# Kernel tuning notes

Hardware: AMD Instinct MI355X
Metric: run time of the kernel (lower is better)

The kernel has to match this reference:

```python
import jax, jax.numpy as jnp
import numpy as np

N, E, T = 32768, 262144, 262144
DN, DE = 128, 128
EPS = 1e-5  # torch LayerNorm default eps


def layer_norm(x, g, b):
    m = jnp.mean(x, axis=-1, keepdims=True)
    v = jnp.mean((x - m) ** 2, axis=-1, keepdims=True)
    return (x - m) * jax.lax.rsqrt(v + EPS) * g + b


def setup_inputs() -> dict:
    key = jax.random.key(0)
    ks = jax.random.split(key, 16)
    node_embedding = jax.random.normal(ks[0], (N, DN), dtype=jnp.float32)
    edge_embedding = jax.random.normal(ks[1], (E, DE), dtype=jnp.float32)
    i = jax.random.randint(ks[2], (E,), 0, N)
    j = jax.random.randint(ks[3], (E,), 0, N)
    index_i = jax.random.randint(ks[4], (T,), 0, N)
    index_j = jax.random.randint(ks[5], (T,), 0, N)
    index_k = jax.random.randint(ks[6], (T,), 0, N)
    index_ji = jax.random.randint(ks[7], (T,), 0, E)
    index_kj = jax.random.randint(ks[8], (T,), 0, E)
    d3 = 3 * DN + 2 * DE
    W2 = jax.random.normal(ks[9], (2 * DE, DN), dtype=jnp.float32) / np.sqrt(DN)
    b2 = jnp.zeros((2 * DE,), dtype=jnp.float32)
    W3 = jax.random.normal(ks[10], (2 * DE, d3), dtype=jnp.float32) / np.sqrt(d3)
    b3 = jnp.zeros((2 * DE,), dtype=jnp.float32)
    g_c2 = jnp.ones((2 * DE,), jnp.float32); be_c2 = jnp.zeros((2 * DE,), jnp.float32)
    g_c3 = jnp.ones((2 * DE,), jnp.float32); be_c3 = jnp.zeros((2 * DE,), jnp.float32)
    g_c2_2 = jnp.ones((DE,), jnp.float32); be_c2_2 = jnp.zeros((DE,), jnp.float32)
    g_c3_2 = jnp.ones((DE,), jnp.float32); be_c3_2 = jnp.zeros((DE,), jnp.float32)
    return dict(node_embedding=node_embedding, edge_embedding=edge_embedding,
                i=i, j=j, index_i=index_i, index_j=index_j, index_k=index_k,
                index_ji=index_ji, index_kj=index_kj,
                W2=W2, b2=b2, W3=W3, b3=b3,
                g_c2=g_c2, be_c2=be_c2, g_c3=g_c3, be_c3=be_c3,
                g_c2_2=g_c2_2, be_c2_2=be_c2_2, g_c3_2=g_c3_2, be_c3_2=be_c3_2)


def reference(node_embedding, edge_embedding, i, j, index_i, index_j, index_k,
              index_ji, index_kj, W2, b2, W3, b3,
              g_c2, be_c2, g_c3, be_c3, g_c2_2, be_c2_2, g_c3_2, be_c3_2):
    num_edges = edge_embedding.shape[0]
    # --- c2 branch: per-edge elementwise product of endpoint node embeddings ---
    c2 = node_embedding[i] * node_embedding[j]                      # [E, Dn]
    c2 = layer_norm(c2 @ W2.T + b2, g_c2, be_c2)                    # [E, 2De]
    c2_filter, c2_core = jnp.split(c2, 2, axis=1)
    c2_emb = layer_norm(jax.nn.sigmoid(c2_filter) * jnp.tanh(c2_core), g_c2_2, be_c2_2)
    # --- c3 branch: triplet gather -> linear -> LN -> gate -> scatter-sum ---
    c3 = jnp.concatenate([node_embedding[index_i], node_embedding[index_j],
                          node_embedding[index_k], edge_embedding[index_ji],
                          edge_embedding[index_kj]], axis=1)        # [T, 3Dn+2De]
    c3 = layer_norm(c3 @ W3.T + b3, g_c3, be_c3)                    # [T, 2De]
    c3_filter, c3_core = jnp.split(c3, 2, axis=1)
    msg = jax.nn.sigmoid(c3_filter) * jnp.tanh(c3_core)             # [T, De]
    c3_emb = jax.ops.segment_sum(msg, index_ji, num_segments=num_edges)  # [E, De]
    c3_emb = layer_norm(c3_emb, g_c3_2, be_c3_2)
    return jnp.tanh(edge_embedding + c2_emb + c3_emb)
```

## Files before the change

### kernel.cpp

```cpp
#include <hip/hip_runtime.h>

typedef _Float16 h16;
typedef _Float16 h16x8 __attribute__((ext_vector_type(8)));
typedef float    f32x4 __attribute__((ext_vector_type(4)));

static constexpr int NN  = 32768;
static constexpr int EE  = 262144;
static constexpr int TT  = 262144;
static constexpr int D   = 128;
static constexpr int K3  = 640;
static constexpr int LDA = 72;
#define EPS 1e-5f

__global__ __launch_bounds__(256) void cvt_f32_f16(
    const float* __restrict__ src, h16* __restrict__ dst, int n8)
{
    const int i = blockIdx.x * 256 + threadIdx.x;
    if (i >= n8) return;
    const float4* s = reinterpret_cast<const float4*>(src);
    const float4 a = s[2 * i], b = s[2 * i + 1];
    h16x8 o;
    o[0] = (h16)a.x; o[1] = (h16)a.y; o[2] = (h16)a.z; o[3] = (h16)a.w;
    o[4] = (h16)b.x; o[5] = (h16)b.y; o[6] = (h16)b.z; o[7] = (h16)b.w;
    *reinterpret_cast<h16x8*>(dst + 8 * i) = o;
}

__global__ __launch_bounds__(256, 2) void c3_kernel(
    const h16*  __restrict__ nodeh, const float* __restrict__ edge,
    const int* __restrict__ idx_i, const int* __restrict__ idx_j,
    const int* __restrict__ idx_k, const int* __restrict__ idx_ji,
    const int* __restrict__ idx_kj,
    const h16* __restrict__ W3h, const float* __restrict__ b3,
    const float* __restrict__ g3, const float* __restrict__ be3,
    float* __restrict__ acc3)
{
    __shared__ h16 As[128 * LDA];
    __shared__ h16 Bs[256 * LDA];

    const int tid  = threadIdx.x;
    const int lane = tid & 63;
    const int wave = tid >> 6;
    const int l15  = lane & 15;
    const int quad = lane >> 4;
    const int m0   = blockIdx.x * 128;

    f32x4 acc[2][16];
    #pragma unroll
    for (int mt = 0; mt < 2; ++mt)
        #pragma unroll
        for (int nt = 0; nt < 16; ++nt)
            acc[mt][nt] = (f32x4){0.f, 0.f, 0.f, 0.f};

    const int r = tid >> 1;
    const int h = tid & 1;

    #pragma unroll 1
    for (int c = 0; c < 10; ++c) {
        const int seg  = c >> 1;
        const int half = c & 1;
        const int* idxarr = (seg == 0) ? idx_i : (seg == 1) ? idx_j
                          : (seg == 2) ? idx_k : (seg == 3) ? idx_ji : idx_kj;
        const size_t row = (size_t)idxarr[m0 + r];
        h16x8 av[4];
        if (seg < 3) {
            const h16x8* sp = reinterpret_cast<const h16x8*>(nodeh + row * D + half * 64 + h * 32);
            #pragma unroll
            for (int q = 0; q < 4; ++q) av[q] = sp[q];
        } else {
            const float4* fp = reinterpret_cast<const float4*>(edge + row * D + half * 64 + h * 32);
            #pragma unroll
            for (int q = 0; q < 4; ++q) {
                const float4 u = fp[2 * q], v = fp[2 * q + 1];
                h16x8 t;
                t[0] = (h16)u.x; t[1] = (h16)u.y; t[2] = (h16)u.z; t[3] = (h16)u.w;
                t[4] = (h16)v.x; t[5] = (h16)v.y; t[6] = (h16)v.z; t[7] = (h16)v.w;
                av[q] = t;
            }
        }
        const h16x8* wp = reinterpret_cast<const h16x8*>(W3h + (size_t)tid * K3 + c * 64);
        h16x8 bv[8];
        #pragma unroll
        for (int q = 0; q < 8; ++q) bv[q] = wp[q];

        __syncthreads();
        h16x8* ad = reinterpret_cast<h16x8*>(&As[r * LDA + h * 32]);
        #pragma unroll
        for (int q = 0; q < 4; ++q) ad[q] = av[q];
        h16x8* bd = reinterpret_cast<h16x8*>(&Bs[tid * LDA]);
        #pragma unroll
        for (int q = 0; q < 8; ++q) bd[q] = bv[q];
        __syncthreads();

        #pragma unroll
        for (int kk = 0; kk < 64; kk += 32) {
            h16x8 a0 = *reinterpret_cast<const h16x8*>(&As[(wave*32      + l15) * LDA + kk + quad*8]);
            h16x8 a1 = *reinterpret_cast<const h16x8*>(&As[(wave*32 + 16 + l15) * LDA + kk + quad*8]);
            #pragma unroll
            for (int nt = 0; nt < 16; ++nt) {
                h16x8 b = *reinterpret_cast<const h16x8*>(&Bs[(nt*16 + l15) * LDA + kk + quad*8]);
                acc[0][nt] = __builtin_amdgcn_mfma_f32_16x16x32_f16(a0, b, acc[0][nt], 0, 0, 0);
                acc[1][nt] = __builtin_amdgcn_mfma_f32_16x16x32_f16(a1, b, acc[1][nt], 0, 0, 0);
            }
        }
    }

    float bias[16], gg[16], bb[16];
    #pragma unroll
    for (int nt = 0; nt < 16; ++nt) {
        const int cc = nt * 16 + l15;
        bias[nt] = b3[cc]; gg[nt] = g3[cc]; bb[nt] = be3[cc];
    }
    #pragma unroll
    for (int mt = 0; mt < 2; ++mt) {
        #pragma unroll
        for (int rg = 0; rg < 4; ++rg) {
            float v[16];
            float s = 0.f, s2 = 0.f;
            #pragma unroll
            for (int nt = 0; nt < 16; ++nt) {
                v[nt] = acc[mt][nt][rg] + bias[nt];
                s += v[nt]; s2 += v[nt] * v[nt];
            }
            #pragma unroll
            for (int m = 1; m < 16; m <<= 1) {
                s  += __shfl_xor(s,  m, 64);
                s2 += __shfl_xor(s2, m, 64);
            }
            const float mean = s * (1.f / 256.f);
            const float var  = s2 * (1.f / 256.f) - mean * mean;
            const float inv  = rsqrtf(var + EPS);
            const int rowg   = m0 + wave * 32 + mt * 16 + quad * 4 + rg;
            const size_t e   = (size_t)idx_ji[rowg];
            #pragma unroll
            for (int nt = 0; nt < 8; ++nt) {
                const float f   = (v[nt]     - mean) * inv * gg[nt]     + bb[nt];
                const float co  = (v[nt + 8] - mean) * inv * gg[nt + 8] + bb[nt + 8];
                const float msg = (1.f / (1.f + __expf(-f))) * tanhf(co);
                atomicAdd(&acc3[e * D + nt * 16 + l15], msg);
            }
        }
    }
}

__global__ __launch_bounds__(256, 2) void c2_kernel(
    const h16* __restrict__ nodeh,
    const int* __restrict__ ei, const int* __restrict__ ej,
    const h16* __restrict__ W2h, const float* __restrict__ b2,
    const float* __restrict__ g2, const float* __restrict__ be2,
    const float* __restrict__ g22, const float* __restrict__ be22,
    h16* __restrict__ c2emb)
{
    __shared__ h16 As[128 * LDA];
    __shared__ h16 Bs[256 * LDA];

    const int tid  = threadIdx.x;
    const int lane = tid & 63;
    const int wave = tid >> 6;
    const int l15  = lane & 15;
    const int quad = lane >> 4;
    const int m0   = blockIdx.x * 128;

    f32x4 acc[2][16];
    #pragma unroll
    for (int mt = 0; mt < 2; ++mt)
        #pragma unroll
        for (int nt = 0; nt < 16; ++nt)
            acc[mt][nt] = (f32x4){0.f, 0.f, 0.f, 0.f};

    const int r = tid >> 1;
    const int h = tid & 1;
    const size_t ri = (size_t)ei[m0 + r];
    const size_t rj = (size_t)ej[m0 + r];

    #pragma unroll 1
    for (int c = 0; c < 2; ++c) {
        const h16x8* si = reinterpret_cast<const h16x8*>(nodeh + ri * D + c * 64 + h * 32);
        const h16x8* sj = reinterpret_cast<const h16x8*>(nodeh + rj * D + c * 64 + h * 32);
        h16x8 av[4];
        #pragma unroll
        for (int q = 0; q < 4; ++q) av[q] = si[q] * sj[q];
        const h16x8* wp = reinterpret_cast<const h16x8*>(W2h + (size_t)tid * D + c * 64);
        h16x8 bv[8];
        #pragma unroll
        for (int q = 0; q < 8; ++q) bv[q] = wp[q];

        __syncthreads();
        h16x8* ad = reinterpret_cast<h16x8*>(&As[r * LDA + h * 32]);
        #pragma unroll
        for (int q = 0; q < 4; ++q) ad[q] = av[q];
        h16x8* bd = reinterpret_cast<h16x8*>(&Bs[tid * LDA]);
        #pragma unroll
        for (int q = 0; q < 8; ++q) bd[q] = bv[q];
        __syncthreads();

        #pragma unroll
        for (int kk = 0; kk < 64; kk += 32) {
            h16x8 a0 = *reinterpret_cast<const h16x8*>(&As[(wave*32      + l15) * LDA + kk + quad*8]);
            h16x8 a1 = *reinterpret_cast<const h16x8*>(&As[(wave*32 + 16 + l15) * LDA + kk + quad*8]);
            #pragma unroll
            for (int nt = 0; nt < 16; ++nt) {
                h16x8 b = *reinterpret_cast<const h16x8*>(&Bs[(nt*16 + l15) * LDA + kk + quad*8]);
                acc[0][nt] = __builtin_amdgcn_mfma_f32_16x16x32_f16(a0, b, acc[0][nt], 0, 0, 0);
                acc[1][nt] = __builtin_amdgcn_mfma_f32_16x16x32_f16(a1, b, acc[1][nt], 0, 0, 0);
            }
        }
    }

    float bias[16], gg[16], bb[16];
    #pragma unroll
    for (int nt = 0; nt < 16; ++nt) {
        const int cc = nt * 16 + l15;
        bias[nt] = b2[cc]; gg[nt] = g2[cc]; bb[nt] = be2[cc];
    }
    float g2c[8], b2c[8];
    #pragma unroll
    for (int nt = 0; nt < 8; ++nt) {
        const int cc = nt * 16 + l15;
        g2c[nt] = g22[cc]; b2c[nt] = be22[cc];
    }
    #pragma unroll
    for (int mt = 0; mt < 2; ++mt) {
        #pragma unroll
        for (int rg = 0; rg < 4; ++rg) {
            float v[16];
            float s = 0.f, s2 = 0.f;
            #pragma unroll
            for (int nt = 0; nt < 16; ++nt) {
                v[nt] = acc[mt][nt][rg] + bias[nt];
                s += v[nt]; s2 += v[nt] * v[nt];
            }
            #pragma unroll
            for (int m = 1; m < 16; m <<= 1) {
                s  += __shfl_xor(s,  m, 64);
                s2 += __shfl_xor(s2, m, 64);
            }
            const float mean = s * (1.f / 256.f);
            const float var  = s2 * (1.f / 256.f) - mean * mean;
            const float inv  = rsqrtf(var + EPS);
            float msg[8];
            float t = 0.f, t2 = 0.f;
            #pragma unroll
            for (int nt = 0; nt < 8; ++nt) {
                const float f  = (v[nt]     - mean) * inv * gg[nt]     + bb[nt];
                const float co = (v[nt + 8] - mean) * inv * gg[nt + 8] + bb[nt + 8];
                const float m_ = (1.f / (1.f + __expf(-f))) * tanhf(co);
                msg[nt] = m_; t += m_; t2 += m_ * m_;
            }
            #pragma unroll
            for (int m = 1; m < 16; m <<= 1) {
                t  += __shfl_xor(t,  m, 64);
                t2 += __shfl_xor(t2, m, 64);
            }
            const float mean2 = t * (1.f / 128.f);
            const float var2  = t2 * (1.f / 128.f) - mean2 * mean2;
            const float inv2  = rsqrtf(var2 + EPS);
            const size_t rowg = (size_t)(m0 + wave * 32 + mt * 16 + quad * 4 + rg);
            #pragma unroll
            for (int nt = 0; nt < 8; ++nt) {
                const float o = (msg[nt] - mean2) * inv2 * g2c[nt] + b2c[nt];
                c2emb[rowg * D + nt * 16 + l15] = (h16)o;
            }
        }
    }
}

__global__ __launch_bounds__(256) void final_kernel(
    const float* __restrict__ edge, const h16* __restrict__ c2emb,
    const float* __restrict__ g32, const float* __restrict__ be32,
    float* out)
{
    const int lane = threadIdx.x & 63;
    const int wave = threadIdx.x >> 6;
    const size_t e = (size_t)blockIdx.x * 4 + wave;
    const int c0 = lane * 2;

    const float2 v = *reinterpret_cast<const float2*>(&out[e * D + c0]);
    float s  = v.x + v.y;
    float s2 = v.x * v.x + v.y * v.y;
    #pragma unroll
    for (int m = 1; m < 64; m <<= 1) {
        s  += __shfl_xor(s,  m, 64);
        s2 += __shfl_xor(s2, m, 64);
    }
    const float mean = s * (1.f / 128.f);
    const float var  = s2 * (1.f / 128.f) - mean * mean;
    const float inv  = rsqrtf(var + EPS);
    const float c3a = (v.x - mean) * inv * g32[c0]     + be32[c0];
    const float c3b = (v.y - mean) * inv * g32[c0 + 1] + be32[c0 + 1];

    const float2 ev = *reinterpret_cast<const float2*>(&edge[e * D + c0]);
    const float ca = (float)c2emb[e * D + c0];
    const float cb = (float)c2emb[e * D + c0 + 1];
    float2 o;
    o.x = tanhf(ev.x + ca + c3a);
    o.y = tanhf(ev.y + cb + c3b);
    *reinterpret_cast<float2*>(&out[e * D + c0]) = o;
}

extern "C" void kernel_launch(void* const* d_in, const int* in_sizes, int n_in,
                              void* d_out, int out_size, void* d_ws, size_t ws_size,
                              hipStream_t stream)
{
    const float* node   = (const float*)d_in[0];
    const float* edge   = (const float*)d_in[1];
    const int*   e_i    = (const int*)d_in[2];
    const int*   e_j    = (const int*)d_in[3];
    const int*   idx_i  = (const int*)d_in[4];
    const int*   idx_j  = (const int*)d_in[5];
    const int*   idx_k  = (const int*)d_in[6];
    const int*   idx_ji = (const int*)d_in[7];
    const int*   idx_kj = (const int*)d_in[8];
    const float* W2     = (const float*)d_in[9];
    const float* b2     = (const float*)d_in[10];
    const float* W3     = (const float*)d_in[11];
    const float* b3     = (const float*)d_in[12];
    const float* g_c2   = (const float*)d_in[13];
    const float* be_c2  = (const float*)d_in[14];
    const float* g_c3   = (const float*)d_in[15];
    const float* be_c3  = (const float*)d_in[16];
    const float* g_c22  = (const float*)d_in[17];
    const float* be_c22 = (const float*)d_in[18];
    const float* g_c32  = (const float*)d_in[19];
    const float* be_c32 = (const float*)d_in[20];

    h16* W3h   = (h16*)d_ws;
    h16* W2h   = W3h + 256 * K3;
    h16* nodeh = W2h + 256 * D;
    h16* c2emb = nodeh + (size_t)NN * D;
    float* acc3 = (float*)d_out;
    float* out  = (float*)d_out;

    hipMemsetAsync(d_out, 0, (size_t)EE * D * sizeof(float), stream);
    cvt_f32_f16<<<dim3((256 * K3 / 8 + 255) / 256), dim3(256), 0, stream>>>(W3, W3h, 256 * K3 / 8);
    cvt_f32_f16<<<dim3((256 * D  / 8 + 255) / 256), dim3(256), 0, stream>>>(W2, W2h, 256 * D / 8);
    cvt_f32_f16<<<dim3((NN * D   / 8 + 255) / 256), dim3(256), 0, stream>>>(node, nodeh, NN * D / 8);

    c3_kernel<<<dim3(TT / 128), dim3(256), 0, stream>>>(
        nodeh, edge, idx_i, idx_j, idx_k, idx_ji, idx_kj, W3h, b3, g_c3, be_c3, acc3);
    c2_kernel<<<dim3(EE / 128), dim3(256), 0, stream>>>(
        nodeh, e_i, e_j, W2h, b2, g_c2, be_c2, g_c22, be_c22, c2emb);
    final_kernel<<<dim3(EE / 4), dim3(256), 0, stream>>>(
        edge, c2emb, g_c32, be_c32, out);
}
```

Baseline: 697.3 us.

## Prefetch next K-chunk into registers and pre-convert edge embeddings to fp16

The c3 and c2 GEMM loops now issue the global loads for the next K-chunk into registers right after the shared-memory store barrier, so gather latency overlaps the MFMA work on the current chunk. The c3 kernel also hoists its five index loads out of the loop. When the workspace is large enough, a new conversion pass turns the edge embeddings into an fp16 copy so the c3 gather reads half the bytes with no per-element conversion. The costs are one extra full pass over the edge tensor, more live registers at the 2-waves-per-SIMD launch bound, and a runtime fallback branch on workspace size.

```diff
diff --git a/kernel.cpp b/kernel.cpp
--- a/kernel.cpp
+++ b/kernel.cpp
@@ -27,6 +27,7 @@
 
 __global__ __launch_bounds__(256, 2) void c3_kernel(
     const h16*  __restrict__ nodeh, const float* __restrict__ edge,
+    const h16*  __restrict__ edgeh,
     const int* __restrict__ idx_i, const int* __restrict__ idx_j,
     const int* __restrict__ idx_k, const int* __restrict__ idx_ji,
     const int* __restrict__ idx_kj,
@@ -54,34 +55,52 @@
     const int r = tid >> 1;
     const int h = tid & 1;
 
+    const size_t rI  = (size_t)idx_i [m0 + r];
+    const size_t rJ  = (size_t)idx_j [m0 + r];
+    const size_t rK  = (size_t)idx_k [m0 + r];
+    const size_t rJI = (size_t)idx_ji[m0 + r];
+    const size_t rKJ = (size_t)idx_kj[m0 + r];
+
+    h16x8 av[4], bv[8];
+
+#define LDC3(c)                                                                          \
+    {                                                                                    \
+        const int seg  = (c) >> 1;                                                       \
+        const int half = (c) & 1;                                                        \
+        const size_t row = (seg == 0) ? rI : (seg == 1) ? rJ                             \
+                         : (seg == 2) ? rK : (seg == 3) ? rJI : rKJ;                     \
+        if (seg < 3) {                                                                   \
+            const h16x8* sp = reinterpret_cast<const h16x8*>(                            \
+                nodeh + row * D + half * 64 + h * 32);                                   \
+            _Pragma("unroll")                                                            \
+            for (int q = 0; q < 4; ++q) av[q] = sp[q];                                   \
+        } else if (edgeh) {                                                              \
+            const h16x8* sp = reinterpret_cast<const h16x8*>(                            \
+                edgeh + row * D + half * 64 + h * 32);                                   \
+            _Pragma("unroll")                                                            \
+            for (int q = 0; q < 4; ++q) av[q] = sp[q];                                   \
+        } else {                                                                         \
+            const float4* fp = reinterpret_cast<const float4*>(                          \
+                edge + row * D + half * 64 + h * 32);                                    \
+            _Pragma("unroll")                                                            \
+            for (int q = 0; q < 4; ++q) {                                                \
+                const float4 u = fp[2 * q], vv = fp[2 * q + 1];                          \
+                h16x8 t;                                                                 \
+                t[0] = (h16)u.x;  t[1] = (h16)u.y;  t[2] = (h16)u.z;  t[3] = (h16)u.w;   \
+                t[4] = (h16)vv.x; t[5] = (h16)vv.y; t[6] = (h16)vv.z; t[7] = (h16)vv.w;  \
+                av[q] = t;                                                               \
+            }                                                                            \
+        }                                                                                \
+        const h16x8* wp = reinterpret_cast<const h16x8*>(                                \
+            W3h + (size_t)tid * K3 + (c) * 64);                                          \
+        _Pragma("unroll")                                                                \
+        for (int q = 0; q < 8; ++q) bv[q] = wp[q];                                       \
+    }
+
+    LDC3(0);
+
     #pragma unroll 1
     for (int c = 0; c < 10; ++c) {
-        const int seg  = c >> 1;
-        const int half = c & 1;
-        const int* idxarr = (seg == 0) ? idx_i : (seg == 1) ? idx_j
-                          : (seg == 2) ? idx_k : (seg == 3) ? idx_ji : idx_kj;
-        const size_t row = (size_t)idxarr[m0 + r];
-        h16x8 av[4];
-        if (seg < 3) {
-            const h16x8* sp = reinterpret_cast<const h16x8*>(nodeh + row * D + half * 64 + h * 32);
-            #pragma unroll
-            for (int q = 0; q < 4; ++q) av[q] = sp[q];
-        } else {
-            const float4* fp = reinterpret_cast<const float4*>(edge + row * D + half * 64 + h * 32);
-            #pragma unroll
-            for (int q = 0; q < 4; ++q) {
-                const float4 u = fp[2 * q], v = fp[2 * q + 1];
-                h16x8 t;
-                t[0] = (h16)u.x; t[1] = (h16)u.y; t[2] = (h16)u.z; t[3] = (h16)u.w;
-                t[4] = (h16)v.x; t[5] = (h16)v.y; t[6] = (h16)v.z; t[7] = (h16)v.w;
-                av[q] = t;
-            }
-        }
-        const h16x8* wp = reinterpret_cast<const h16x8*>(W3h + (size_t)tid * K3 + c * 64);
-        h16x8 bv[8];
-        #pragma unroll
-        for (int q = 0; q < 8; ++q) bv[q] = wp[q];
-
         __syncthreads();
         h16x8* ad = reinterpret_cast<h16x8*>(&As[r * LDA + h * 32]);
         #pragma unroll
@@ -90,6 +109,8 @@
         #pragma unroll
         for (int q = 0; q < 8; ++q) bd[q] = bv[q];
         __syncthreads();
+
+        if (c < 9) LDC3(c + 1);
 
         #pragma unroll
         for (int kk = 0; kk < 64; kk += 32) {
@@ -103,6 +124,7 @@
             }
         }
     }
+#undef LDC3
 
     float bias[16], gg[16], bb[16];
     #pragma unroll
@@ -172,18 +194,26 @@
     const size_t ri = (size_t)ei[m0 + r];
     const size_t rj = (size_t)ej[m0 + r];
 
+    h16x8 av[4], bv[8];
+
+#define LDC2(c)                                                                          \
+    {                                                                                    \
+        const h16x8* si = reinterpret_cast<const h16x8*>(                                \
+            nodeh + ri * D + (c) * 64 + h * 32);                                         \
+        const h16x8* sj = reinterpret_cast<const h16x8*>(                                \
+            nodeh + rj * D + (c) * 64 + h * 32);                                         \
+        _Pragma("unroll")                                                                \
+        for (int q = 0; q < 4; ++q) av[q] = si[q] * sj[q];                               \
+        const h16x8* wp = reinterpret_cast<const h16x8*>(                                \
+            W2h + (size_t)tid * D + (c) * 64);                                           \
+        _Pragma("unroll")                                                                \
+        for (int q = 0; q < 8; ++q) bv[q] = wp[q];                                       \
+    }
+
+    LDC2(0);
+
     #pragma unroll 1
     for (int c = 0; c < 2; ++c) {
-        const h16x8* si = reinterpret_cast<const h16x8*>(nodeh + ri * D + c * 64 + h * 32);
-        const h16x8* sj = reinterpret_cast<const h16x8*>(nodeh + rj * D + c * 64 + h * 32);
-        h16x8 av[4];
-        #pragma unroll
-        for (int q = 0; q < 4; ++q) av[q] = si[q] * sj[q];
-        const h16x8* wp = reinterpret_cast<const h16x8*>(W2h + (size_t)tid * D + c * 64);
-        h16x8 bv[8];
-        #pragma unroll
-        for (int q = 0; q < 8; ++q) bv[q] = wp[q];
-
         __syncthreads();
         h16x8* ad = reinterpret_cast<h16x8*>(&As[r * LDA + h * 32]);
         #pragma unroll
@@ -192,6 +222,8 @@
         #pragma unroll
         for (int q = 0; q < 8; ++q) bd[q] = bv[q];
         __syncthreads();
+
+        if (c < 1) LDC2(c + 1);
 
         #pragma unroll
         for (int kk = 0; kk < 64; kk += 32) {
@@ -205,6 +237,7 @@
             }
         }
     }
+#undef LDC2
 
     float bias[16], gg[16], bb[16];
     #pragma unroll
@@ -327,6 +360,11 @@
     h16* W2h   = W3h + 256 * K3;
     h16* nodeh = W2h + 256 * D;
     h16* c2emb = nodeh + (size_t)NN * D;
+    h16* edgeh = c2emb + (size_t)EE * D;
+    const size_t need = ((size_t)256 * K3 + 256 * D + (size_t)NN * D
+                         + 2 * (size_t)EE * D) * sizeof(h16);
+    const bool use_edgeh = ws_size >= need;
+
     float* acc3 = (float*)d_out;
     float* out  = (float*)d_out;
 
@@ -334,9 +372,12 @@
     cvt_f32_f16<<<dim3((256 * K3 / 8 + 255) / 256), dim3(256), 0, stream>>>(W3, W3h, 256 * K3 / 8);
     cvt_f32_f16<<<dim3((256 * D  / 8 + 255) / 256), dim3(256), 0, stream>>>(W2, W2h, 256 * D / 8);
     cvt_f32_f16<<<dim3((NN * D   / 8 + 255) / 256), dim3(256), 0, stream>>>(node, nodeh, NN * D / 8);
+    if (use_edgeh)
+        cvt_f32_f16<<<dim3((EE * D / 8 + 255) / 256), dim3(256), 0, stream>>>(edge, edgeh, EE * D / 8);
 
     c3_kernel<<<dim3(TT / 128), dim3(256), 0, stream>>>(
-        nodeh, edge, idx_i, idx_j, idx_k, idx_ji, idx_kj, W3h, b3, g_c3, be_c3, acc3);
+        nodeh, edge, use_edgeh ? edgeh : (const h16*)nullptr,
+        idx_i, idx_j, idx_k, idx_ji, idx_kj, W3h, b3, g_c3, be_c3, acc3);
     c2_kernel<<<dim3(EE / 128), dim3(256), 0, stream>>>(
         nodeh, e_i, e_j, W2h, b2, g_c2, be_c2, g_c22, be_c22, c2emb);
     final_kernel<<<dim3(EE / 4), dim3(256), 0, stream>>>(
```

Result: no change. 688.9 us (-1.2%).
